# Optimization experiments

Measured on AMD Instinct MI355X. Metric: run time of the kernel, lower is better.

The kernel has to match this reference:

```python
import jax, jax.numpy as jnp
import numpy as np

N_NODES = 50000
N_EDGES = 800000
DIM = 128
NEG_SLOPE = 0.01  # nn.LeakyReLU default


def setup_inputs() -> dict:
    key = jax.random.key(0)
    ks = jax.random.split(key, 9)
    src = jax.random.randint(ks[0], (N_EDGES,), 0, N_NODES, dtype=jnp.int32)
    dst = jax.random.randint(ks[1], (N_EDGES,), 0, N_NODES, dtype=jnp.int32)
    weight = jax.random.normal(ks[2], (N_NODES,), dtype=jnp.float32)
    significance = jax.random.randint(ks[3], (N_NODES,), 0, 2, dtype=jnp.int32)
    emb = jax.random.normal(ks[4], (2, 2), dtype=jnp.float32) * 0.1
    W0 = jax.random.normal(ks[5], (3, DIM), dtype=jnp.float32) * (1.0 / np.sqrt(3))
    b0 = jnp.zeros((DIM,), dtype=jnp.float32)
    W1 = jax.random.normal(ks[6], (DIM, DIM), dtype=jnp.float32) * (1.0 / np.sqrt(DIM))
    b1 = jnp.zeros((DIM,), dtype=jnp.float32)
    return {"src": src, "dst": dst, "weight": weight, "significance": significance,
            "emb": emb, "W0": W0, "b0": b0, "W1": W1, "b1": b1}


def _graph_conv(src, dst, x, W, b, n_nodes):
    # DGL GraphConv, norm='both', allow_zero_in_degree=True:
    # h = D_in^{-1/2} A D_out^{-1/2} x W + b, degrees clamped to >= 1.
    ones = jnp.ones(src.shape[0], dtype=x.dtype)
    out_deg = jnp.clip(jax.ops.segment_sum(ones, src, num_segments=n_nodes), 1.0)
    in_deg = jnp.clip(jax.ops.segment_sum(ones, dst, num_segments=n_nodes), 1.0)
    h = x * (out_deg ** -0.5)[:, None]            # [N, d] scale src side
    agg = jax.ops.segment_sum(h[src], dst, num_segments=n_nodes)  # gather+scatter over edges
    agg = agg * (in_deg ** -0.5)[:, None]
    return agg @ W + b


def reference(src, dst, weight, significance, emb, W0, b0, W1, b1):
    n_nodes = weight.shape[0]
    sig = emb[significance]                        # [N, 2] embedding lookup
    feats = jnp.concatenate([weight[:, None], sig], axis=1)  # [N, 3]
    h = _graph_conv(src, dst, feats, W0, b0, n_nodes)        # conv_0
    h = jax.nn.leaky_relu(h, negative_slope=NEG_SLOPE)
    h = _graph_conv(src, dst, h, W1, b1, n_nodes)            # layers[0]
    return h
```

## Files before the change

### kernel.cpp

```cpp
#include <hip/hip_runtime.h>

#define N_NODES 50000
#define N_EDGES 800000
#define DIM 128
#define NEG_SLOPE 0.01f
#define CAP 32
#define OVF_MAX 4096

#define NR 4
#define RNODES 12512
#define SLICES 64
#define ESLICE (N_EDGES / SLICES)

__device__ inline unsigned f2b_rne2(float a, float b) {
    unsigned ua = __float_as_uint(a), ub = __float_as_uint(b);
    ua = (ua + 0x7fffu + ((ua >> 16) & 1u)) >> 16;
    ub = (ub + 0x7fffu + ((ub >> 16) & 1u)) >> 16;
    return ua | (ub << 16);
}
__device__ inline float b2f_lo(unsigned u) { return __uint_as_float(u << 16); }
__device__ inline float b2f_hi(unsigned u) { return __uint_as_float(u & 0xffff0000u); }

__global__ __launch_bounds__(512) void k_hist2(const int* __restrict__ src,
                                               const int* __restrict__ dst,
                                               int* __restrict__ pSrc, int* __restrict__ pDst) {
    __shared__ int bs[RNODES];
    __shared__ int bd[RNODES];
    int range = blockIdx.x / SLICES;
    int slice = blockIdx.x % SLICES;
    int tid = threadIdx.x;
    for (int j = tid; j < RNODES; j += 512) { bs[j] = 0; bd[j] = 0; }
    __syncthreads();
    int base = range * RNODES;
    const int4* s4 = (const int4*)(src + slice * ESLICE);
    const int4* d4 = (const int4*)(dst + slice * ESLICE);
    for (int t = tid; t < ESLICE / 4; t += 512) {
        int4 v = s4[t];
        unsigned u0 = (unsigned)(v.x - base), u1 = (unsigned)(v.y - base);
        unsigned u2 = (unsigned)(v.z - base), u3 = (unsigned)(v.w - base);
        if (u0 < RNODES) atomicAdd(&bs[u0], 1);
        if (u1 < RNODES) atomicAdd(&bs[u1], 1);
        if (u2 < RNODES) atomicAdd(&bs[u2], 1);
        if (u3 < RNODES) atomicAdd(&bs[u3], 1);
        int4 w = d4[t];
        unsigned w0 = (unsigned)(w.x - base), w1 = (unsigned)(w.y - base);
        unsigned w2 = (unsigned)(w.z - base), w3 = (unsigned)(w.w - base);
        if (w0 < RNODES) atomicAdd(&bd[w0], 1);
        if (w1 < RNODES) atomicAdd(&bd[w1], 1);
        if (w2 < RNODES) atomicAdd(&bd[w2], 1);
        if (w3 < RNODES) atomicAdd(&bd[w3], 1);
    }
    __syncthreads();
    int* os = pSrc + (size_t)blockIdx.x * RNODES;
    int* od = pDst + (size_t)blockIdx.x * RNODES;
    for (int j = tid; j < RNODES; j += 512) { os[j] = bs[j]; od[j] = bd[j]; }
}

__global__ void k_scanprep(const float* __restrict__ weight, const int* __restrict__ sig,
                           const float* __restrict__ emb,
                           const int* __restrict__ pSrc, int* __restrict__ pDst,
                           int* __restrict__ icnt, float* __restrict__ oinv,
                           float* __restrict__ iinv, float* __restrict__ feats3,
                           int* __restrict__ ovf_cnt, int n) {
    int g = blockIdx.x * blockDim.x + threadIdx.x;
    if (g == 0) *ovf_cnt = 0;
    if (g >= NR * RNODES) return;
    int range = g / RNODES, off = g % RNODES;
    size_t basei = (size_t)(range * SLICES) * RNODES + off;
    int run = 0;
    #pragma unroll 8
    for (int s = 0; s < SLICES; ++s) {
        size_t idx = basei + (size_t)s * RNODES;
        int c = pDst[idx];
        pDst[idx] = run;
        run += c;
    }
    int od = 0;
    #pragma unroll 8
    for (int s = 0; s < SLICES; ++s) od += pSrc[basei + (size_t)s * RNODES];
    if (g < n) {
        icnt[g] = run;
        float oi = 1.0f / sqrtf((float)max(od, 1));
        oinv[g] = oi;
        iinv[g] = 1.0f / sqrtf((float)max(run, 1));
        int sg = sig[g];
        feats3[g * 3 + 0] = weight[g] * oi;
        feats3[g * 3 + 1] = emb[sg * 2 + 0] * oi;
        feats3[g * 3 + 2] = emb[sg * 2 + 1] * oi;
    }
}

__global__ __launch_bounds__(512) void k_fill3(const int* __restrict__ src,
                                               const int* __restrict__ dst,
                                               const int* __restrict__ pDst,
                                               unsigned short* __restrict__ eidx,
                                               int* __restrict__ ovf_cnt, int2* __restrict__ ovf) {
    __shared__ int cur[RNODES];
    int range = blockIdx.x / SLICES;
    int slice = blockIdx.x % SLICES;
    int tid = threadIdx.x;
    const int* pr = pDst + (size_t)blockIdx.x * RNODES;
    for (int j = tid; j < RNODES; j += 512) cur[j] = pr[j];
    __syncthreads();
    int base = range * RNODES;
    const int* ss = src + slice * ESLICE;
    const int* dd = dst + slice * ESLICE;
    for (int t = tid; t < ESLICE; t += 512) {
        int d = dd[t];
        unsigned u = (unsigned)(d - base);
        if (u < RNODES) {
            int s = ss[t];
            int p = atomicAdd(&cur[u], 1);
            if (p < CAP) eidx[(size_t)d * CAP + p] = (unsigned short)s;
            else { int o = atomicAdd(ovf_cnt, 1); if (o < OVF_MAX) ovf[o] = make_int2(d, s); }
        }
    }
}

__global__ void k_aggl1(const int* __restrict__ icnt, const unsigned short* __restrict__ eidx,
                        const float* __restrict__ feats3,
                        const int* __restrict__ ovf_cnt, const int2* __restrict__ ovf,
                        const float* __restrict__ iinv, const float* __restrict__ oinv,
                        const float* __restrict__ W0, const float* __restrict__ b0,
                        unsigned* __restrict__ hs, int n) {
    int t = blockIdx.x * blockDim.x + threadIdx.x;
    int i = t >> 5;
    if (i >= n) return;
    int q = t & 31;
    int ic = icnt[i];
    int deg = min(ic, CAP);
    const unsigned short* row = eidx + (size_t)i * CAP;
    float a0 = 0.f, a1 = 0.f, a2 = 0.f;
    for (int k = q; k < deg; k += 32) {
        int s = row[k];
        a0 += feats3[s * 3 + 0];
        a1 += feats3[s * 3 + 1];
        a2 += feats3[s * 3 + 2];
    }
    if (ic > CAP) {
        int cnt = min(*ovf_cnt, OVF_MAX);
        for (int e = q; e < cnt; e += 32) {
            int2 ov = ovf[e];
            if (ov.x == i) {
                a0 += feats3[ov.y * 3 + 0];
                a1 += feats3[ov.y * 3 + 1];
                a2 += feats3[ov.y * 3 + 2];
            }
        }
    }
    #pragma unroll
    for (int m = 1; m <= 16; m <<= 1) {
        a0 += __shfl_xor(a0, m);
        a1 += __shfl_xor(a1, m);
        a2 += __shfl_xor(a2, m);
    }
    float ii = iinv[i], oi = oinv[i];
    a0 *= ii; a1 *= ii; a2 *= ii;
    int j0 = q * 4;
    float4 w0r = *(const float4*)&W0[0 * DIM + j0];
    float4 w1r = *(const float4*)&W0[1 * DIM + j0];
    float4 w2r = *(const float4*)&W0[2 * DIM + j0];
    float4 bb  = *(const float4*)&b0[j0];
    float v0 = a0 * w0r.x + a1 * w1r.x + a2 * w2r.x + bb.x;
    float v1 = a0 * w0r.y + a1 * w1r.y + a2 * w2r.y + bb.y;
    float v2 = a0 * w0r.z + a1 * w1r.z + a2 * w2r.z + bb.z;
    float v3 = a0 * w0r.w + a1 * w1r.w + a2 * w2r.w + bb.w;
    v0 = v0 > 0.f ? v0 : NEG_SLOPE * v0;
    v1 = v1 > 0.f ? v1 : NEG_SLOPE * v1;
    v2 = v2 > 0.f ? v2 : NEG_SLOPE * v2;
    v3 = v3 > 0.f ? v3 : NEG_SLOPE * v3;
    ((uint2*)hs)[i * 32 + q] = make_uint2(f2b_rne2(v0 * oi, v1 * oi),
                                          f2b_rne2(v2 * oi, v3 * oi));
}

__global__ void k_gather128(const int* __restrict__ icnt, const unsigned short* __restrict__ eidx,
                            const unsigned* __restrict__ hs,
                            const int* __restrict__ ovf_cnt, const int2* __restrict__ ovf,
                            float* __restrict__ agg, int n) {
    int t = blockIdx.x * blockDim.x + threadIdx.x;
    int i = t >> 5;
    if (i >= n) return;
    int q = t & 31;
    int ic = icnt[i];
    int deg = min(ic, CAP);
    const unsigned short* row = eidx + (size_t)i * CAP;
    const uint2* hs2 = (const uint2*)hs;
    float a0 = 0.f, a1 = 0.f, a2 = 0.f, a3 = 0.f;
    int k = 0;
    for (; k + 8 <= deg; k += 8) {
        int s0 = row[k + 0], s1 = row[k + 1], s2 = row[k + 2], s3 = row[k + 3];
        int s4 = row[k + 4], s5 = row[k + 5], s6 = row[k + 6], s7 = row[k + 7];
        uint2 u0 = hs2[s0 * 32 + q];
        uint2 u1 = hs2[s1 * 32 + q];
        uint2 u2 = hs2[s2 * 32 + q];
        uint2 u3 = hs2[s3 * 32 + q];
        uint2 u4 = hs2[s4 * 32 + q];
        uint2 u5 = hs2[s5 * 32 + q];
        uint2 u6 = hs2[s6 * 32 + q];
        uint2 u7 = hs2[s7 * 32 + q];
        a0 += (b2f_lo(u0.x) + b2f_lo(u1.x)) + (b2f_lo(u2.x) + b2f_lo(u3.x))
            + (b2f_lo(u4.x) + b2f_lo(u5.x)) + (b2f_lo(u6.x) + b2f_lo(u7.x));
        a1 += (b2f_hi(u0.x) + b2f_hi(u1.x)) + (b2f_hi(u2.x) + b2f_hi(u3.x))
            + (b2f_hi(u4.x) + b2f_hi(u5.x)) + (b2f_hi(u6.x) + b2f_hi(u7.x));
        a2 += (b2f_lo(u0.y) + b2f_lo(u1.y)) + (b2f_lo(u2.y) + b2f_lo(u3.y))
            + (b2f_lo(u4.y) + b2f_lo(u5.y)) + (b2f_lo(u6.y) + b2f_lo(u7.y));
        a3 += (b2f_hi(u0.y) + b2f_hi(u1.y)) + (b2f_hi(u2.y) + b2f_hi(u3.y))
            + (b2f_hi(u4.y) + b2f_hi(u5.y)) + (b2f_hi(u6.y) + b2f_hi(u7.y));
    }
    for (; k + 2 <= deg; k += 2) {
        int s0 = row[k], s1 = row[k + 1];
        uint2 u0 = hs2[s0 * 32 + q];
        uint2 u1 = hs2[s1 * 32 + q];
        a0 += b2f_lo(u0.x) + b2f_lo(u1.x);
        a1 += b2f_hi(u0.x) + b2f_hi(u1.x);
        a2 += b2f_lo(u0.y) + b2f_lo(u1.y);
        a3 += b2f_hi(u0.y) + b2f_hi(u1.y);
    }
    if (k < deg) {
        int s = row[k];
        uint2 u = hs2[s * 32 + q];
        a0 += b2f_lo(u.x); a1 += b2f_hi(u.x);
        a2 += b2f_lo(u.y); a3 += b2f_hi(u.y);
    }
    if (ic > CAP) {
        int cnt = min(*ovf_cnt, OVF_MAX);
        for (int e = 0; e < cnt; ++e) {
            int2 ov = ovf[e];
            if (ov.x == i) {
                uint2 u = hs2[ov.y * 32 + q];
                a0 += b2f_lo(u.x); a1 += b2f_hi(u.x);
                a2 += b2f_lo(u.y); a3 += b2f_hi(u.y);
            }
        }
    }
    ((float4*)agg)[i * 32 + q] = make_float4(a0, a1, a2, a3);
}

#define FB_NODES 256
__global__ __launch_bounds__(256) void k_final(const float* __restrict__ iinv,
                                               const float* __restrict__ W1,
                                               const float* __restrict__ b1,
                                               const float* __restrict__ agg,
                                               float* __restrict__ out, int n) {
    __shared__ float sW[DIM * 64];
    int tid = threadIdx.x;
    int half = blockIdx.x & 1;
    int tile = blockIdx.x >> 1;
    for (int idx = tid; idx < DIM * 64 / 4; idx += 256) {
        int r = idx >> 4, c4 = idx & 15;
        *(float4*)&sW[r * 64 + c4 * 4] = *(const float4*)&W1[r * DIM + half * 64 + c4 * 4];
    }
    int cg = tid & 7;
    int ng = tid >> 3;
    int col0 = cg * 8;
    int row0 = tile * FB_NODES + ng * 8;

    float acc[8][8];
    #pragma unroll
    for (int i = 0; i < 8; ++i)
        #pragma unroll
        for (int j = 0; j < 8; ++j) acc[i][j] = 0.f;

    __syncthreads();

    const float4* agg4 = (const float4*)agg;
    for (int k4 = 0; k4 < 32; ++k4) {
        float4 a[8];
        #pragma unroll
        for (int i = 0; i < 8; ++i) {
            int r = min(row0 + i, n - 1);
            a[i] = agg4[(size_t)r * 32 + k4];
        }
        #pragma unroll
        for (int kk = 0; kk < 4; ++kk) {
            float4 w0 = *(const float4*)&sW[(k4 * 4 + kk) * 64 + col0];
            float4 w1v = *(const float4*)&sW[(k4 * 4 + kk) * 64 + col0 + 4];
            #pragma unroll
            for (int i = 0; i < 8; ++i) {
                float av = (kk == 0) ? a[i].x : (kk == 1) ? a[i].y : (kk == 2) ? a[i].z : a[i].w;
                acc[i][0] += av * w0.x;  acc[i][1] += av * w0.y;
                acc[i][2] += av * w0.z;  acc[i][3] += av * w0.w;
                acc[i][4] += av * w1v.x; acc[i][5] += av * w1v.y;
                acc[i][6] += av * w1v.z; acc[i][7] += av * w1v.w;
            }
        }
    }

    int gcol = half * 64 + col0;
    float4 bb0 = *(const float4*)&b1[gcol];
    float4 bb1 = *(const float4*)&b1[gcol + 4];
    #pragma unroll
    for (int i = 0; i < 8; ++i) {
        int r = row0 + i;
        if (r < n) {
            float ii = iinv[r];
            float4 o0, o1;
            o0.x = acc[i][0] * ii + bb0.x; o0.y = acc[i][1] * ii + bb0.y;
            o0.z = acc[i][2] * ii + bb0.z; o0.w = acc[i][3] * ii + bb0.w;
            o1.x = acc[i][4] * ii + bb1.x; o1.y = acc[i][5] * ii + bb1.y;
            o1.z = acc[i][6] * ii + bb1.z; o1.w = acc[i][7] * ii + bb1.w;
            ((float4*)out)[(size_t)r * 32 + (gcol >> 2)] = o0;
            ((float4*)out)[(size_t)r * 32 + (gcol >> 2) + 1] = o1;
        }
    }
}

extern "C" void kernel_launch(void* const* d_in, const int* in_sizes, int n_in,
                              void* d_out, int out_size, void* d_ws, size_t ws_size,
                              hipStream_t stream) {
    const int*   src  = (const int*)d_in[0];
    const int*   dst  = (const int*)d_in[1];
    const float* weight = (const float*)d_in[2];
    const int*   sig  = (const int*)d_in[3];
    const float* emb  = (const float*)d_in[4];
    const float* W0   = (const float*)d_in[5];
    const float* b0   = (const float*)d_in[6];
    const float* W1   = (const float*)d_in[7];
    const float* b1   = (const float*)d_in[8];
    float* out = (float*)d_out;

    int*   ovf_cnt = (int*)d_ws;
    int2*  ovf     = (int2*)(ovf_cnt + 8);
    int*   icnt    = (int*)(ovf + OVF_MAX);
    float* oinv    = (float*)(icnt + N_NODES);
    float* iinv    = oinv + N_NODES;
    float* feats3  = iinv + N_NODES;
    int*   pSrc    = (int*)(feats3 + 3 * N_NODES);
    int*   pDst    = pSrc + (size_t)NR * SLICES * RNODES;
    unsigned short* eidx = (unsigned short*)(pDst + (size_t)NR * SLICES * RNODES);
    unsigned* hs   = (unsigned*)(eidx + (size_t)N_NODES * CAP);
    float* aggbuf  = (float*)(hs + (size_t)N_NODES * 64);

    k_hist2<<<NR * SLICES, 512, 0, stream>>>(src, dst, pSrc, pDst);
    k_scanprep<<<(NR * RNODES + 255) / 256, 256, 0, stream>>>(weight, sig, emb, pSrc, pDst,
                                                              icnt, oinv, iinv, feats3,
                                                              ovf_cnt, N_NODES);
    k_fill3<<<NR * SLICES, 512, 0, stream>>>(src, dst, pDst, eidx, ovf_cnt, ovf);
    k_aggl1<<<(N_NODES * 32 + 255) / 256, 256, 0, stream>>>(icnt, eidx, feats3,
                                                            ovf_cnt, ovf, iinv, oinv,
                                                            W0, b0, hs, N_NODES);
    k_gather128<<<((N_NODES * 32) + 255) / 256, 256, 0, stream>>>(icnt, eidx, hs,
                                                                  ovf_cnt, ovf, aggbuf,
                                                                  N_NODES);
    k_final<<<((N_NODES + FB_NODES - 1) / FB_NODES) * 2, 256, 0, stream>>>(
        iinv, W1, b1, aggbuf, out, N_NODES);
}
```

Before: 127.4 us.

## Widen gathers to 16-lane uint4 per node and shrink final GEMM tile

Layer-1 aggregation and the 128-wide gather now use 16 lanes per node, each moving a uint4 (8 bf16 values), instead of 32 lanes each moving a uint2. This halves the number of gather instructions and threads per node and aims to improve memory-level parallelism per load. The final GEMM kernel now uses 128-node tiles with 4 output columns per thread, which lowers register pressure and doubles the block count, at the cost of more shared-memory reads per FMA. The degree tail loop is simplified to a single-step loop.

```diff
diff --git a/kernel.cpp b/kernel.cpp
--- a/kernel.cpp
+++ b/kernel.cpp
@@ -122,16 +122,16 @@
                         const int* __restrict__ ovf_cnt, const int2* __restrict__ ovf,
                         const float* __restrict__ iinv, const float* __restrict__ oinv,
                         const float* __restrict__ W0, const float* __restrict__ b0,
-                        unsigned* __restrict__ hs, int n) {
+                        uint4* __restrict__ hs, int n) {
     int t = blockIdx.x * blockDim.x + threadIdx.x;
-    int i = t >> 5;
+    int i = t >> 4;
     if (i >= n) return;
-    int q = t & 31;
+    int q = t & 15;
     int ic = icnt[i];
     int deg = min(ic, CAP);
     const unsigned short* row = eidx + (size_t)i * CAP;
     float a0 = 0.f, a1 = 0.f, a2 = 0.f;
-    for (int k = q; k < deg; k += 32) {
+    for (int k = q; k < deg; k += 16) {
         int s = row[k];
         a0 += feats3[s * 3 + 0];
         a1 += feats3[s * 3 + 1];
@@ -139,7 +139,7 @@
     }
     if (ic > CAP) {
         int cnt = min(*ovf_cnt, OVF_MAX);
-        for (int e = q; e < cnt; e += 32) {
+        for (int e = q; e < cnt; e += 16) {
             int2 ov = ovf[e];
             if (ov.x == i) {
                 a0 += feats3[ov.y * 3 + 0];
@@ -149,55 +149,52 @@
         }
     }
     #pragma unroll
-    for (int m = 1; m <= 16; m <<= 1) {
+    for (int m = 1; m <= 8; m <<= 1) {
         a0 += __shfl_xor(a0, m);
         a1 += __shfl_xor(a1, m);
         a2 += __shfl_xor(a2, m);
     }
     float ii = iinv[i], oi = oinv[i];
     a0 *= ii; a1 *= ii; a2 *= ii;
-    int j0 = q * 4;
-    float4 w0r = *(const float4*)&W0[0 * DIM + j0];
-    float4 w1r = *(const float4*)&W0[1 * DIM + j0];
-    float4 w2r = *(const float4*)&W0[2 * DIM + j0];
-    float4 bb  = *(const float4*)&b0[j0];
-    float v0 = a0 * w0r.x + a1 * w1r.x + a2 * w2r.x + bb.x;
-    float v1 = a0 * w0r.y + a1 * w1r.y + a2 * w2r.y + bb.y;
-    float v2 = a0 * w0r.z + a1 * w1r.z + a2 * w2r.z + bb.z;
-    float v3 = a0 * w0r.w + a1 * w1r.w + a2 * w2r.w + bb.w;
-    v0 = v0 > 0.f ? v0 : NEG_SLOPE * v0;
-    v1 = v1 > 0.f ? v1 : NEG_SLOPE * v1;
-    v2 = v2 > 0.f ? v2 : NEG_SLOPE * v2;
-    v3 = v3 > 0.f ? v3 : NEG_SLOPE * v3;
-    ((uint2*)hs)[i * 32 + q] = make_uint2(f2b_rne2(v0 * oi, v1 * oi),
-                                          f2b_rne2(v2 * oi, v3 * oi));
+    int j0 = q * 8;
+    float v[8];
+    #pragma unroll
+    for (int c = 0; c < 8; ++c) {
+        float x = a0 * W0[j0 + c] + a1 * W0[DIM + j0 + c] + a2 * W0[2 * DIM + j0 + c]
+                + b0[j0 + c];
+        v[c] = x > 0.f ? x : NEG_SLOPE * x;
+    }
+    hs[i * 16 + q] = make_uint4(f2b_rne2(v[0] * oi, v[1] * oi),
+                                f2b_rne2(v[2] * oi, v[3] * oi),
+                                f2b_rne2(v[4] * oi, v[5] * oi),
+                                f2b_rne2(v[6] * oi, v[7] * oi));
 }
 
 __global__ void k_gather128(const int* __restrict__ icnt, const unsigned short* __restrict__ eidx,
-                            const unsigned* __restrict__ hs,
+                            const uint4* __restrict__ hs,
                             const int* __restrict__ ovf_cnt, const int2* __restrict__ ovf,
                             float* __restrict__ agg, int n) {
     int t = blockIdx.x * blockDim.x + threadIdx.x;
-    int i = t >> 5;
+    int i = t >> 4;
     if (i >= n) return;
-    int q = t & 31;
+    int q = t & 15;
     int ic = icnt[i];
     int deg = min(ic, CAP);
     const unsigned short* row = eidx + (size_t)i * CAP;
-    const uint2* hs2 = (const uint2*)hs;
     float a0 = 0.f, a1 = 0.f, a2 = 0.f, a3 = 0.f;
+    float a4 = 0.f, a5 = 0.f, a6 = 0.f, a7 = 0.f;
     int k = 0;
     for (; k + 8 <= deg; k += 8) {
         int s0 = row[k + 0], s1 = row[k + 1], s2 = row[k + 2], s3 = row[k + 3];
         int s4 = row[k + 4], s5 = row[k + 5], s6 = row[k + 6], s7 = row[k + 7];
-        uint2 u0 = hs2[s0 * 32 + q];
-        uint2 u1 = hs2[s1 * 32 + q];
-        uint2 u2 = hs2[s2 * 32 + q];
-        uint2 u3 = hs2[s3 * 32 + q];
-        uint2 u4 = hs2[s4 * 32 + q];
-        uint2 u5 = hs2[s5 * 32 + q];
-        uint2 u6 = hs2[s6 * 32 + q];
-        uint2 u7 = hs2[s7 * 32 + q];
+        uint4 u0 = hs[s0 * 16 + q];
+        uint4 u1 = hs[s1 * 16 + q];
+        uint4 u2 = hs[s2 * 16 + q];
+        uint4 u3 = hs[s3 * 16 + q];
+        uint4 u4 = hs[s4 * 16 + q];
+        uint4 u5 = hs[s5 * 16 + q];
+        uint4 u6 = hs[s6 * 16 + q];
+        uint4 u7 = hs[s7 * 16 + q];
         a0 += (b2f_lo(u0.x) + b2f_lo(u1.x)) + (b2f_lo(u2.x) + b2f_lo(u3.x))
             + (b2f_lo(u4.x) + b2f_lo(u5.x)) + (b2f_lo(u6.x) + b2f_lo(u7.x));
         a1 += (b2f_hi(u0.x) + b2f_hi(u1.x)) + (b2f_hi(u2.x) + b2f_hi(u3.x))
@@ -206,37 +203,41 @@
             + (b2f_lo(u4.y) + b2f_lo(u5.y)) + (b2f_lo(u6.y) + b2f_lo(u7.y));
         a3 += (b2f_hi(u0.y) + b2f_hi(u1.y)) + (b2f_hi(u2.y) + b2f_hi(u3.y))
             + (b2f_hi(u4.y) + b2f_hi(u5.y)) + (b2f_hi(u6.y) + b2f_hi(u7.y));
-    }
-    for (; k + 2 <= deg; k += 2) {
-        int s0 = row[k], s1 = row[k + 1];
-        uint2 u0 = hs2[s0 * 32 + q];
-        uint2 u1 = hs2[s1 * 32 + q];
-        a0 += b2f_lo(u0.x) + b2f_lo(u1.x);
-        a1 += b2f_hi(u0.x) + b2f_hi(u1.x);
-        a2 += b2f_lo(u0.y) + b2f_lo(u1.y);
-        a3 += b2f_hi(u0.y) + b2f_hi(u1.y);
-    }
-    if (k < deg) {
+        a4 += (b2f_lo(u0.z) + b2f_lo(u1.z)) + (b2f_lo(u2.z) + b2f_lo(u3.z))
+            + (b2f_lo(u4.z) + b2f_lo(u5.z)) + (b2f_lo(u6.z) + b2f_lo(u7.z));
+        a5 += (b2f_hi(u0.z) + b2f_hi(u1.z)) + (b2f_hi(u2.z) + b2f_hi(u3.z))
+            + (b2f_hi(u4.z) + b2f_hi(u5.z)) + (b2f_hi(u6.z) + b2f_hi(u7.z));
+        a6 += (b2f_lo(u0.w) + b2f_lo(u1.w)) + (b2f_lo(u2.w) + b2f_lo(u3.w))
+            + (b2f_lo(u4.w) + b2f_lo(u5.w)) + (b2f_lo(u6.w) + b2f_lo(u7.w));
+        a7 += (b2f_hi(u0.w) + b2f_hi(u1.w)) + (b2f_hi(u2.w) + b2f_hi(u3.w))
+            + (b2f_hi(u4.w) + b2f_hi(u5.w)) + (b2f_hi(u6.w) + b2f_hi(u7.w));
+    }
+    for (; k < deg; ++k) {
         int s = row[k];
-        uint2 u = hs2[s * 32 + q];
+        uint4 u = hs[s * 16 + q];
         a0 += b2f_lo(u.x); a1 += b2f_hi(u.x);
         a2 += b2f_lo(u.y); a3 += b2f_hi(u.y);
+        a4 += b2f_lo(u.z); a5 += b2f_hi(u.z);
+        a6 += b2f_lo(u.w); a7 += b2f_hi(u.w);
     }
     if (ic > CAP) {
         int cnt = min(*ovf_cnt, OVF_MAX);
         for (int e = 0; e < cnt; ++e) {
             int2 ov = ovf[e];
             if (ov.x == i) {
-                uint2 u = hs2[ov.y * 32 + q];
+                uint4 u = hs[ov.y * 16 + q];
                 a0 += b2f_lo(u.x); a1 += b2f_hi(u.x);
                 a2 += b2f_lo(u.y); a3 += b2f_hi(u.y);
+                a4 += b2f_lo(u.z); a5 += b2f_hi(u.z);
+                a6 += b2f_lo(u.w); a7 += b2f_hi(u.w);
             }
         }
     }
-    ((float4*)agg)[i * 32 + q] = make_float4(a0, a1, a2, a3);
-}
-
-#define FB_NODES 256
+    ((float4*)agg)[(size_t)i * 32 + q * 2 + 0] = make_float4(a0, a1, a2, a3);
+    ((float4*)agg)[(size_t)i * 32 + q * 2 + 1] = make_float4(a4, a5, a6, a7);
+}
+
+#define FB_NODES 128
 __global__ __launch_bounds__(256) void k_final(const float* __restrict__ iinv,
                                                const float* __restrict__ W1,
                                                const float* __restrict__ b1,
@@ -250,20 +251,21 @@
         int r = idx >> 4, c4 = idx & 15;
         *(float4*)&sW[r * 64 + c4 * 4] = *(const float4*)&W1[r * DIM + half * 64 + c4 * 4];
     }
-    int cg = tid & 7;
-    int ng = tid >> 3;
-    int col0 = cg * 8;
+    int cg = tid & 15;
+    int ng = tid >> 4;
+    int col0 = cg * 4;
     int row0 = tile * FB_NODES + ng * 8;
 
-    float acc[8][8];
+    float acc[8][4];
     #pragma unroll
     for (int i = 0; i < 8; ++i)
         #pragma unroll
-        for (int j = 0; j < 8; ++j) acc[i][j] = 0.f;
+        for (int j = 0; j < 4; ++j) acc[i][j] = 0.f;
 
     __syncthreads();
 
     const float4* agg4 = (const float4*)agg;
+    #pragma unroll 2
     for (int k4 = 0; k4 < 32; ++k4) {
         float4 a[8];
         #pragma unroll
@@ -273,34 +275,31 @@
         }
         #pragma unroll
         for (int kk = 0; kk < 4; ++kk) {
-            float4 w0 = *(const float4*)&sW[(k4 * 4 + kk) * 64 + col0];
-            float4 w1v = *(const float4*)&sW[(k4 * 4 + kk) * 64 + col0 + 4];
+            float4 w = *(const float4*)&sW[(k4 * 4 + kk) * 64 + col0];
             #pragma unroll
             for (int i = 0; i < 8; ++i) {
                 float av = (kk == 0) ? a[i].x : (kk == 1) ? a[i].y : (kk == 2) ? a[i].z : a[i].w;
-                acc[i][0] += av * w0.x;  acc[i][1] += av * w0.y;
-                acc[i][2] += av * w0.z;  acc[i][3] += av * w0.w;
-                acc[i][4] += av * w1v.x; acc[i][5] += av * w1v.y;
-                acc[i][6] += av * w1v.z; acc[i][7] += av * w1v.w;
+                acc[i][0] += av * w.x;
+                acc[i][1] += av * w.y;
+                acc[i][2] += av * w.z;
+                acc[i][3] += av * w.w;
             }
         }
     }
 
     int gcol = half * 64 + col0;
-    float4 bb0 = *(const float4*)&b1[gcol];
-    float4 bb1 = *(const float4*)&b1[gcol + 4];
+    float4 bb = *(const float4*)&b1[gcol];
     #pragma unroll
     for (int i = 0; i < 8; ++i) {
         int r = row0 + i;
         if (r < n) {
             float ii = iinv[r];
-            float4 o0, o1;
-            o0.x = acc[i][0] * ii + bb0.x; o0.y = acc[i][1] * ii + bb0.y;
-            o0.z = acc[i][2] * ii + bb0.z; o0.w = acc[i][3] * ii + bb0.w;
-            o1.x = acc[i][4] * ii + bb1.x; o1.y = acc[i][5] * ii + bb1.y;
-            o1.z = acc[i][6] * ii + bb1.z; o1.w = acc[i][7] * ii + bb1.w;
-            ((float4*)out)[(size_t)r * 32 + (gcol >> 2)] = o0;
-            ((float4*)out)[(size_t)r * 32 + (gcol >> 2) + 1] = o1;
+            float4 o;
+            o.x = acc[i][0] * ii + bb.x;
+            o.y = acc[i][1] * ii + bb.y;
+            o.z = acc[i][2] * ii + bb.z;
+            o.w = acc[i][3] * ii + bb.w;
+            ((float4*)out)[(size_t)r * 32 + (gcol >> 2)] = o;
         }
     }
 }
@@ -328,18 +327,18 @@
     int*   pSrc    = (int*)(feats3 + 3 * N_NODES);
     int*   pDst    = pSrc + (size_t)NR * SLICES * RNODES;
     unsigned short* eidx = (unsigned short*)(pDst + (size_t)NR * SLICES * RNODES);
-    unsigned* hs   = (unsigned*)(eidx + (size_t)N_NODES * CAP);
-    float* aggbuf  = (float*)(hs + (size_t)N_NODES * 64);
+    uint4* hs      = (uint4*)(eidx + (size_t)N_NODES * CAP);
+    float* aggbuf  = (float*)(hs + (size_t)N_NODES * 16);
 
     k_hist2<<<NR * SLICES, 512, 0, stream>>>(src, dst, pSrc, pDst);
     k_scanprep<<<(NR * RNODES + 255) / 256, 256, 0, stream>>>(weight, sig, emb, pSrc, pDst,
                                                               icnt, oinv, iinv, feats3,
                                                               ovf_cnt, N_NODES);
     k_fill3<<<NR * SLICES, 512, 0, stream>>>(src, dst, pDst, eidx, ovf_cnt, ovf);
-    k_aggl1<<<(N_NODES * 32 + 255) / 256, 256, 0, stream>>>(icnt, eidx, feats3,
+    k_aggl1<<<(N_NODES * 16 + 255) / 256, 256, 0, stream>>>(icnt, eidx, feats3,
                                                             ovf_cnt, ovf, iinv, oinv,
                                                             W0, b0, hs, N_NODES);
-    k_gather128<<<((N_NODES * 32) + 255) / 256, 256, 0, stream>>>(icnt, eidx, hs,
+    k_gather128<<<((N_NODES * 16) + 255) / 256, 256, 0, stream>>>(icnt, eidx, hs,
                                                                   ovf_cnt, ovf, aggbuf,
                                                                   N_NODES);
     k_final<<<((N_NODES + FB_NODES - 1) / FB_NODES) * 2, 256, 0, stream>>>(
```

Result: slower. 137.4 us (+7.8%).
